# Kernel tuning notes

Hardware: AMD Instinct MI355X
Metric: run time of the kernel (lower is better)

The kernel has to match this reference:

```python
import jax, jax.numpy as jnp
import numpy as np

EPS = 1e-5

def _fftfreq(n, d):
    k = jnp.concatenate([jnp.arange(0, (n + 1) // 2), jnp.arange(-(n // 2), 0)]).astype(jnp.float32)
    return k / (n * d)

def _inorm(x):
    # InstanceNorm2d, no affine, biased variance, eps=1e-5; x: (B,C,H,W)
    m = jnp.mean(x, axis=(-2, -1), keepdims=True)
    v = jnp.var(x, axis=(-2, -1), keepdims=True)
    return (x - m) / jnp.sqrt(v + EPS)

def _spectral_conv(x, t_grid, x_grid, p1, p2, res):
    # x: (B, C, Sx, Sy) real; p1:(in,out,m1) p2:(in,out,m2) res:(in,out,m1,m2) complex64
    B, C, Sx, Sy = x.shape
    dty = x_grid[0, 1] - x_grid[0, 0]
    dtx = t_grid[0, 1] - t_grid[0, 0]
    alpha = jnp.fft.fft2(x, axes=(-2, -1))  # (B,in,Sx,Sy) complex
    om1 = (_fftfreq(Sx, dty) * (2 * jnp.pi) * 1j).astype(jnp.complex64)  # (Sx,)
    om2 = (_fftfreq(Sy, dtx) * (2 * jnp.pi) * 1j).astype(jnp.complex64)  # (Sy,)
    d1 = om1[:, None, None, None] - p1  # (Sx,in,out,m1)
    d2 = om2[:, None, None, None] - p2  # (Sy,in,out,m2)
    denom = jnp.einsum('pbix,qbik->pqbixk', d1, d2)  # (Sx,Sy,in,out,m1,m2)
    Hw = res[None, None] / denom  # pole-residue rational kernel
    r1 = jnp.einsum('biox,oxikpq->bkox', alpha, Hw)  # (B,out,Sx,Sy)
    r2 = jnp.einsum('biox,oxikpq->bkpq', alpha, Hw)  # (B,out,m1,m2)
    x1 = jnp.real(jnp.fft.ifft2(r1, s=(Sx, Sy), axes=(-2, -1)))
    ty_c = x_grid.reshape(1, -1).astype(jnp.complex64)  # (1,Sx)
    tx_c = t_grid.reshape(1, -1).astype(jnp.complex64)  # (1,Sy)
    e1 = jnp.exp(jnp.einsum('bip,kz->bipz', p1, ty_c))  # (in,out,m1,Sx)
    e2 = jnp.exp(jnp.einsum('biq,kx->biqx', p2, tx_c))  # (in,out,m2,Sy)
    term3 = jnp.einsum('bipz,biqx->bipqzx', e1, e2)     # (in,out,m1,m2,Sx,Sy)
    x2 = jnp.real(jnp.einsum('kbpq,bipqzx->kizx', r2, term3)) / (Sx * Sy)
    return x1 + x2

def reference(x, fc0_w, fc0_b, p1r, p1i, p2r, p2i, resr, resi,
              w0_w, w0_b, fc1_w, fc1_b, fc2_w, fc2_b, t_grid, x_grid):
    B, Sx, Sy, _ = x.shape
    gx = jnp.broadcast_to(jnp.linspace(0.0, 1.0, Sx, dtype=jnp.float32)[None, :, None, None], (B, Sx, Sy, 1))
    gy = jnp.broadcast_to(jnp.linspace(0.0, 1.0, Sy, dtype=jnp.float32)[None, None, :, None], (B, Sx, Sy, 1))
    h = jnp.concatenate([x, gx, gy], axis=-1)           # (B,Sx,Sy,3)
    h = h @ fc0_w.T + fc0_b                              # (B,Sx,Sy,16)
    h = h.transpose(0, 3, 1, 2)                          # (B,16,Sx,Sy)
    p1 = (p1r + 1j * p1i).astype(jnp.complex64)
    p2 = (p2r + 1j * p2i).astype(jnp.complex64)
    res = (resr + 1j * resi).astype(jnp.complex64)
    x1 = _inorm(_spectral_conv(_inorm(h), t_grid, x_grid, p1, p2, res))
    x2 = jnp.einsum('bihw,oi->bohw', h, w0_w) + w0_b[None, :, None, None]  # 1x1 conv
    h = x1 + x2
    h = h.transpose(0, 2, 3, 1)                          # (B,Sx,Sy,16)
    h = jnp.sin(h @ fc1_w.T + fc1_b)                     # (B,Sx,Sy,128)
    h = h @ fc2_w.T + fc2_b                              # (B,Sx,Sy,1)
    return h

def setup_inputs() -> dict:
    key = jax.random.key(0)
    ks = jax.random.split(key, 16)
    W, M1, M2, B, S = 16, 4, 5, 4, 64
    scale = 1.0 / (W * W)
    inp = {
        'x': jax.random.normal(ks[0], (B, S, S, 1), jnp.float32),
        'fc0_w': jax.random.normal(ks[1], (W, 3), jnp.float32) * 0.3,
        'fc0_b': jax.random.normal(ks[2], (W,), jnp.float32) * 0.1,
        'p1r': jax.random.uniform(ks[3], (W, W, M1), jnp.float32) * scale,
        'p1i': jax.random.uniform(ks[4], (W, W, M1), jnp.float32) * scale,
        'p2r': jax.random.uniform(ks[5], (W, W, M2), jnp.float32) * scale,
        'p2i': jax.random.uniform(ks[6], (W, W, M2), jnp.float32) * scale,
        'resr': jax.random.uniform(ks[7], (W, W, M1, M2), jnp.float32) * scale,
        'resi': jax.random.uniform(ks[8], (W, W, M1, M2), jnp.float32) * scale,
        'w0_w': jax.random.normal(ks[9], (W, W), jnp.float32) * 0.25,
        'w0_b': jax.random.normal(ks[10], (W,), jnp.float32) * 0.1,
        'fc1_w': jax.random.normal(ks[11], (128, W), jnp.float32) * 0.25,
        'fc1_b': jax.random.normal(ks[12], (128,), jnp.float32) * 0.1,
        'fc2_w': jax.random.normal(ks[13], (1, 128), jnp.float32) * 0.1,
        'fc2_b': jax.random.normal(ks[14], (1,), jnp.float32) * 0.1,
        't_grid': jnp.linspace(0.0, 1.0, S, dtype=jnp.float32).reshape(1, S),
        'x_grid': jnp.linspace(0.0, 1.0, S, dtype=jnp.float32).reshape(1, S),
    }
    return inp
```

## Files before the change

### kernel.cpp

```cpp
#include <hip/hip_runtime.h>

typedef float2 cplx;

constexpr int NPIX = 4096;
constexpr float TWO_PI = 6.28318530717958647692f;

__device__ inline void cmac(float& ax, float& ay, cplx a, cplx b) {
    ax += a.x * b.x - a.y * b.y;
    ay += a.x * b.y + a.y * b.x;
}

__global__ __launch_bounds__(256) void k_pre(
    const float* __restrict__ p1r, const float* __restrict__ p1i,
    const float* __restrict__ p2r, const float* __restrict__ p2i,
    const float* __restrict__ resr, const float* __restrict__ resi,
    const float* __restrict__ t_grid, const float* __restrict__ x_grid,
    cplx* __restrict__ A, cplx* __restrict__ Bq, cplx* __restrict__ Cq,
    cplx* __restrict__ e1, cplx* __restrict__ e2)
{
    int idx = blockIdx.x * 256 + threadIdx.x;
    float dty = x_grid[1] - x_grid[0];
    float dtx = t_grid[1] - t_grid[0];
    const int NA = 65536, NBQ = 81920, NCQ = 81920, NE1 = 65536;
    if (idx < NA) {
        int p = idx & 3, k = (idx >> 2) & 15, i = (idx >> 6) & 15, o = idx >> 10;
        int kf = (o < 32) ? o : o - 64;
        float om = TWO_PI * (float)kf / (64.f * dty);
        float dr = -p1r[(i * 16 + k) * 4 + p], di = om - p1i[(i * 16 + k) * 4 + p];
        float inv = 1.f / (dr * dr + di * di);
        A[idx] = make_float2(dr * inv, -di * inv);
        return;
    }
    idx -= NA;
    if (idx < NBQ) {
        int q = idx % 5, k = (idx / 5) & 15, i = (idx / 80) & 15, xx = idx / 1280;
        int kf = (xx < 32) ? xx : xx - 64;
        float om = TWO_PI * (float)kf / (64.f * dtx);
        float dr = -p2r[(i * 16 + k) * 5 + q], di = om - p2i[(i * 16 + k) * 5 + q];
        float inv = 1.f / (dr * dr + di * di);
        Bq[idx] = make_float2(dr * inv, -di * inv);
        return;
    }
    idx -= NBQ;
    if (idx < NCQ) {
        int q = idx % 5, k = (idx / 5) & 15, i = (idx / 80) & 15, o = idx / 1280;
        int kf = (o < 32) ? o : o - 64;
        float om = TWO_PI * (float)kf / (64.f * dty);
        float cx = 0.f, cy = 0.f;
        for (int p = 0; p < 4; ++p) {
            float dr = -p1r[(i * 16 + k) * 4 + p], di = om - p1i[(i * 16 + k) * 4 + p];
            float inv = 1.f / (dr * dr + di * di);
            float axr = dr * inv, axi = -di * inv;
            float rr = resr[((i * 16 + k) * 4 + p) * 5 + q];
            float ri = resi[((i * 16 + k) * 4 + p) * 5 + q];
            cx += rr * axr - ri * axi;
            cy += rr * axi + ri * axr;
        }
        Cq[idx] = make_float2(cx, cy);
        return;
    }
    idx -= NCQ;
    if (idx < NE1) {
        int z = idx & 63, w = idx >> 6;
        float t = x_grid[z];
        float m = expf(p1r[w] * t);
        float sn, cs; sincosf(p1i[w] * t, &sn, &cs);
        e1[idx] = make_float2(m * cs, m * sn);
        return;
    }
    idx -= NE1;
    {
        int xx = idx & 63, w = idx >> 6;
        float t = t_grid[xx];
        float m = expf(p2r[w] * t);
        float sn, cs; sincosf(p2i[w] * t, &sn, &cs);
        e2[idx] = make_float2(m * cs, m * sn);
    }
}

__global__ __launch_bounds__(1024) void k1_h_norm_fftA(
    const float* __restrict__ x, const float* __restrict__ fc0_w,
    const float* __restrict__ fc0_b, float* __restrict__ h, cplx* __restrict__ T1)
{
    __shared__ float tile[4096];
    __shared__ float rs[32];
    __shared__ cplx Ws[64];
    int bc = blockIdx.x, b = bc >> 4, c = bc & 15;
    int tid = threadIdx.x;
    if (tid < 64) { float sn, cs; sincosf(-TWO_PI * tid / 64.f, &sn, &cs); Ws[tid] = make_float2(cs, sn); }
    float w0 = fc0_w[c * 3], w1 = fc0_w[c * 3 + 1], w2 = fc0_w[c * 3 + 2], bb = fc0_b[c];
    const float inv63 = 1.f / 63.f;
    float vals[4]; float s = 0.f;
    for (int t = 0; t < 4; ++t) {
        int pix = t * 1024 + tid; int z = pix >> 6, xx = pix & 63;
        float v = w0 * x[b * 4096 + pix] + w1 * (z * inv63) + w2 * (xx * inv63) + bb;
        vals[t] = v; s += v; h[bc * 4096 + pix] = v;
    }
    for (int m = 32; m; m >>= 1) s += __shfl_xor(s, m, 64);
    if ((tid & 63) == 0) rs[tid >> 6] = s;
    __syncthreads();
    if (tid == 0) { float t0 = 0; for (int w = 0; w < 16; ++w) t0 += rs[w]; rs[16] = t0; }
    __syncthreads();
    float mean = rs[16] * (1.f / 4096.f);
    float s2 = 0.f;
    for (int t = 0; t < 4; ++t) { float d = vals[t] - mean; s2 += d * d; }
    for (int m = 32; m; m >>= 1) s2 += __shfl_xor(s2, m, 64);
    __syncthreads();
    if ((tid & 63) == 0) rs[tid >> 6] = s2;
    __syncthreads();
    if (tid == 0) { float t0 = 0; for (int w = 0; w < 16; ++w) t0 += rs[w]; rs[16] = t0; }
    __syncthreads();
    float rstd = rsqrtf(rs[16] * (1.f / 4096.f) + 1e-5f);
    for (int t = 0; t < 4; ++t) { int pix = t * 1024 + tid; tile[pix] = (vals[t] - mean) * rstd; }
    __syncthreads();
    int j = tid & 63, pl = tid >> 6;
    for (int t = 0; t < 4; ++t) {
        int p = pl + t * 16;
        float ax = 0.f, ay = 0.f;
        #pragma unroll 8
        for (int i = 0; i < 64; ++i) {
            float v = tile[i * 64 + j];
            cplx w = Ws[(p * i) & 63];
            ax += v * w.x; ay += v * w.y;
        }
        T1[bc * 4096 + p * 64 + j] = make_float2(ax, ay);
    }
}

__global__ __launch_bounds__(256) void k2_fftB(
    const cplx* __restrict__ T1, cplx* __restrict__ alpha, cplx* __restrict__ alphaT)
{
    __shared__ cplx T1s[256];
    __shared__ cplx Ws[64];
    int bc = blockIdx.x >> 4, pc = blockIdx.x & 15;
    int tid = threadIdx.x;
    if (tid < 64) { float sn, cs; sincosf(-TWO_PI * tid / 64.f, &sn, &cs); Ws[tid] = make_float2(cs, sn); }
    T1s[tid] = T1[bc * 4096 + pc * 256 + tid];
    __syncthreads();
    int q = tid & 63, pl = tid >> 6, p = pc * 4 + pl;
    float ax = 0.f, ay = 0.f;
    #pragma unroll 8
    for (int j = 0; j < 64; ++j) cmac(ax, ay, T1s[pl * 64 + j], Ws[(q * j) & 63]);
    cplx v = make_float2(ax, ay);
    alpha [bc * 4096 + p * 64 + q] = v;
    alphaT[(p * 64 + q) * 64 + bc] = v;
}

__global__ __launch_bounds__(64) void k3_r1(
    const cplx* __restrict__ alphaT, const cplx* __restrict__ Cq,
    const cplx* __restrict__ Bq, cplx* __restrict__ r1)
{
    __shared__ cplx Cqs[1280], Bqs[1280], Gs[256], as[64];
    int ox = blockIdx.x; int o = ox >> 6, xx = ox & 63;
    int t = threadIdx.x;
    for (int m = 0; m < 20; ++m) {
        Cqs[m * 64 + t] = Cq[o * 1280 + m * 64 + t];
        Bqs[m * 64 + t] = Bq[xx * 1280 + m * 64 + t];
    }
    as[t] = alphaT[ox * 64 + t];
    __syncthreads();
    for (int m = 0; m < 4; ++m) {
        int e = m * 64 + t; int i = e >> 4, k = e & 15;
        float gx = 0.f, gy = 0.f;
        for (int q = 0; q < 5; ++q) cmac(gx, gy, Cqs[i * 80 + k * 5 + q], Bqs[i * 80 + k * 5 + q]);
        Gs[e] = make_float2(gx, gy);
    }
    __syncthreads();
    int b = t >> 4, k = t & 15;
    float ax = 0.f, ay = 0.f;
    for (int i = 0; i < 16; ++i) cmac(ax, ay, as[b * 16 + i], Gs[i * 16 + k]);
    r1[t * 4096 + ox] = make_float2(ax, ay);
}

__global__ __launch_bounds__(256) void k4_inner1(
    const cplx* __restrict__ alpha, const cplx* __restrict__ Bq,
    cplx* __restrict__ inner1)
{
    int idx = blockIdx.x * 256 + threadIdx.x;
    int kq = idx % 80; int r = idx / 80; int o = r & 63; int bi = r >> 6; int i = bi & 15;
    const cplx* arow = alpha + bi * 4096 + o * 64;
    const cplx* bcol = Bq + i * 80 + kq;
    float ax = 0.f, ay = 0.f;
    #pragma unroll 4
    for (int x = 0; x < 64; ++x) cmac(ax, ay, arow[x], bcol[x * 1280]);
    inner1[idx] = make_float2(ax, ay);
}

__global__ __launch_bounds__(64) void k5_r2(
    const cplx* __restrict__ A, const cplx* __restrict__ inner1,
    const float* __restrict__ resr, const float* __restrict__ resi,
    cplx* __restrict__ r2)
{
    int bk = blockIdx.x; int b = bk >> 4, k = bk & 15;
    int o = threadIdx.x;
    float accx[4][5] = {}, accy[4][5] = {};
    for (int i = 0; i < 16; ++i) {
        cplx a[4];
        for (int p = 0; p < 4; ++p) a[p] = A[((o * 16 + i) * 16 + k) * 4 + p];
        cplx in[5];
        for (int q = 0; q < 5; ++q) in[q] = inner1[(b * 16 + i) * 5120 + o * 80 + k * 5 + q];
        int rb = (i * 16 + k) * 20;
        for (int p = 0; p < 4; ++p)
            for (int q = 0; q < 5; ++q) {
                float tx = a[p].x * in[q].x - a[p].y * in[q].y;
                float ty = a[p].x * in[q].y + a[p].y * in[q].x;
                float rr = resr[rb + p * 5 + q], ri = resi[rb + p * 5 + q];
                accx[p][q] += rr * tx - ri * ty;
                accy[p][q] += rr * ty + ri * tx;
            }
    }
    for (int m = 32; m; m >>= 1)
        for (int p = 0; p < 4; ++p)
            for (int q = 0; q < 5; ++q) {
                accx[p][q] += __shfl_xor(accx[p][q], m, 64);
                accy[p][q] += __shfl_xor(accy[p][q], m, 64);
            }
    if (o == 0)
        for (int p = 0; p < 4; ++p)
            for (int q = 0; q < 5; ++q)
                r2[bk * 20 + p * 5 + q] = make_float2(accx[p][q], accy[p][q]);
}

__global__ __launch_bounds__(256) void k6_V(
    const cplx* __restrict__ r2, const cplx* __restrict__ e1, cplx* __restrict__ V)
{
    int idx = blockIdx.x * 256 + threadIdx.x;
    int z = idx & 63;
    int rest = idx >> 6;
    int q = rest % 5; rest /= 5;
    int bb = rest & 15; rest >>= 4;
    int i = rest & 15;
    int kb = rest >> 4;
    float vx = 0.f, vy = 0.f;
    for (int p = 0; p < 4; ++p)
        cmac(vx, vy, r2[((kb * 16 + bb) * 4 + p) * 5 + q],
                     e1[((bb * 16 + i) * 4 + p) * 64 + z]);
    V[idx] = make_float2(vx, vy);
}

__global__ __launch_bounds__(256) void k7_ifftA(
    const cplx* __restrict__ r1, cplx* __restrict__ T2)
{
    __shared__ cplx Ws[64];
    int bk = blockIdx.x >> 4, zc = blockIdx.x & 15;
    int tid = threadIdx.x;
    if (tid < 64) { float sn, cs; sincosf(TWO_PI * tid / 64.f, &sn, &cs); Ws[tid] = make_float2(cs, sn); }
    __syncthreads();
    int j = tid & 63, z = zc * 4 + (tid >> 6);
    const cplx* rr = r1 + bk * 4096 + j;
    float ax = 0.f, ay = 0.f;
    #pragma unroll 4
    for (int o = 0; o < 64; ++o) cmac(ax, ay, rr[o * 64], Ws[(z * o) & 63]);
    T2[bk * 4096 + z * 64 + j] = make_float2(ax, ay);
}

__global__ __launch_bounds__(1024) void k8_sp(
    const cplx* __restrict__ T2, const cplx* __restrict__ V,
    const cplx* __restrict__ e2, float* __restrict__ spn)
{
    __shared__ cplx Es[5120];
    __shared__ float rs[32];
    __shared__ cplx Ws[64];
    int blk = blockIdx.x;
    int ch = blk & 15;
    int tid = threadIdx.x;
    if (tid < 64) { float sn, cs; sincosf(TWO_PI * tid / 64.f, &sn, &cs); Ws[tid] = make_float2(cs, sn); }
    for (int t = 0; t < 5; ++t) {
        int f = t * 1024 + tid; int xx = f & 63, bq = f >> 6; int bb = bq / 5, q = bq % 5;
        Es[f] = e2[((bb * 16 + ch) * 5 + q) * 64 + xx];
    }
    __syncthreads();
    const cplx* T2b = T2 + blk * 4096;
    const cplx* Vb  = V  + blk * 5120;
    int xx = tid & 63;
    float vals[4]; float s = 0.f;
    for (int t = 0; t < 4; ++t) {
        int pix = t * 1024 + tid; int z = pix >> 6;
        float acc = 0.f;
        const cplx* trow = T2b + z * 64;
        #pragma unroll 4
        for (int j2 = 0; j2 < 64; ++j2) {
            cplx v = trow[j2]; cplx w = Ws[(xx * j2) & 63];
            acc += v.x * w.x - v.y * w.y;
        }
        #pragma unroll 4
        for (int bq = 0; bq < 80; ++bq) {
            cplx vv = Vb[bq * 64 + z];
            cplx ee = Es[bq * 64 + xx];
            acc += vv.x * ee.x - vv.y * ee.y;
        }
        float val = acc * (1.f / 4096.f);
        vals[t] = val; s += val;
    }
    for (int m = 32; m; m >>= 1) s += __shfl_xor(s, m, 64);
    if ((tid & 63) == 0) rs[tid >> 6] = s;
    __syncthreads();
    if (tid == 0) { float t0 = 0; for (int w = 0; w < 16; ++w) t0 += rs[w]; rs[16] = t0; }
    __syncthreads();
    float mean = rs[16] * (1.f / 4096.f);
    float s2 = 0.f;
    for (int t = 0; t < 4; ++t) { float d = vals[t] - mean; s2 += d * d; }
    for (int m = 32; m; m >>= 1) s2 += __shfl_xor(s2, m, 64);
    __syncthreads();
    if ((tid & 63) == 0) rs[tid >> 6] = s2;
    __syncthreads();
    if (tid == 0) { float t0 = 0; for (int w = 0; w < 16; ++w) t0 += rs[w]; rs[16] = t0; }
    __syncthreads();
    float rstd = rsqrtf(rs[16] * (1.f / 4096.f) + 1e-5f);
    for (int t = 0; t < 4; ++t) {
        int pix = t * 1024 + tid;
        spn[blk * 4096 + pix] = (vals[t] - mean) * rstd;
    }
}

__global__ __launch_bounds__(256) void k9_final(
    const float* __restrict__ spn, const float* __restrict__ h,
    const float* __restrict__ w0_w, const float* __restrict__ w0_b,
    const float* __restrict__ fc1_w, const float* __restrict__ fc1_b,
    const float* __restrict__ fc2_w, const float* __restrict__ fc2_b,
    float* __restrict__ out)
{
    __shared__ float w1s[128 * 16], b1s[128], w2s[128], w0s[256], w0bs[16];
    int tid = threadIdx.x;
    for (int t = 0; t < 8; ++t) w1s[t * 256 + tid] = fc1_w[t * 256 + tid];
    if (tid < 128) { b1s[tid] = fc1_b[tid]; w2s[tid] = fc2_w[tid]; }
    w0s[tid] = w0_w[tid & 255];
    if (tid < 16) w0bs[tid] = w0_b[tid];
    float b2 = fc2_b[0];
    __syncthreads();
    int pix = blockIdx.x * 256 + tid;
    int b = pix >> 12, rem = pix & 4095;
    float hv[16], tv[16];
    for (int c = 0; c < 16; ++c) {
        hv[c] = h[(b * 16 + c) * 4096 + rem];
        tv[c] = spn[(b * 16 + c) * 4096 + rem];
    }
    for (int k = 0; k < 16; ++k) {
        float a = w0bs[k];
        for (int c = 0; c < 16; ++c) a += w0s[k * 16 + c] * hv[c];
        tv[k] += a;
    }
    float acc = b2;
    for (int n = 0; n < 128; ++n) {
        float s1 = b1s[n];
        for (int k2 = 0; k2 < 16; ++k2) s1 += w1s[n * 16 + k2] * tv[k2];
        acc += w2s[n] * sinf(s1);
    }
    out[pix] = acc;
}

extern "C" void kernel_launch(void* const* d_in, const int* in_sizes, int n_in,
                              void* d_out, int out_size, void* d_ws, size_t ws_size,
                              hipStream_t stream)
{
    const float* x     = (const float*)d_in[0];
    const float* fc0_w = (const float*)d_in[1];
    const float* fc0_b = (const float*)d_in[2];
    const float* p1r   = (const float*)d_in[3];
    const float* p1i   = (const float*)d_in[4];
    const float* p2r   = (const float*)d_in[5];
    const float* p2i   = (const float*)d_in[6];
    const float* resr  = (const float*)d_in[7];
    const float* resi  = (const float*)d_in[8];
    const float* w0_w  = (const float*)d_in[9];
    const float* w0_b  = (const float*)d_in[10];
    const float* fc1_w = (const float*)d_in[11];
    const float* fc1_b = (const float*)d_in[12];
    const float* fc2_w = (const float*)d_in[13];
    const float* fc2_b = (const float*)d_in[14];
    const float* t_grid= (const float*)d_in[15];
    const float* x_grid= (const float*)d_in[16];
    float* out = (float*)d_out;

    float* ws = (float*)d_ws;
    size_t off = 0;
    float* h      = ws + off; off += 262144;
    cplx*  T1     = (cplx*)(ws + off); off += 524288;
    cplx*  alpha  = (cplx*)(ws + off); off += 524288;
    cplx*  alphaT = (cplx*)(ws + off); off += 524288;
    cplx*  A      = (cplx*)(ws + off); off += 131072;
    cplx*  Bq     = (cplx*)(ws + off); off += 163840;
    cplx*  Cq     = (cplx*)(ws + off); off += 163840;
    cplx*  e1     = (cplx*)(ws + off); off += 131072;
    cplx*  e2     = (cplx*)(ws + off); off += 163840;
    cplx*  r1     = (cplx*)(ws + off); off += 524288;
    cplx*  inner1 = (cplx*)(ws + off); off += 655360;
    cplx*  r2     = (cplx*)(ws + off); off += 2560;
    cplx*  V      = (cplx*)(ws + off); off += 655360;
    cplx*  T2     = (cplx*)(ws + off); off += 524288;
    float* spn    = ws + off; off += 262144;
    (void)ws_size; (void)n_in; (void)in_sizes; (void)out_size;

    k_pre<<<1472, 256, 0, stream>>>(p1r, p1i, p2r, p2i, resr, resi, t_grid, x_grid,
                                    A, Bq, Cq, e1, e2);
    k1_h_norm_fftA<<<64, 1024, 0, stream>>>(x, fc0_w, fc0_b, h, T1);
    k2_fftB<<<1024, 256, 0, stream>>>(T1, alpha, alphaT);
    k3_r1<<<4096, 64, 0, stream>>>(alphaT, Cq, Bq, r1);
    k4_inner1<<<1280, 256, 0, stream>>>(alpha, Bq, inner1);
    k5_r2<<<64, 64, 0, stream>>>(A, inner1, resr, resi, r2);
    k6_V<<<1280, 256, 0, stream>>>(r2, e1, V);
    k7_ifftA<<<1024, 256, 0, stream>>>(r1, T2);
    k8_sp<<<64, 1024, 0, stream>>>(T2, V, e2, spn);
    k9_final<<<64, 256, 0, stream>>>(spn, h, w0_w, w0_b, fc1_w, fc1_b, fc2_w, fc2_b, out);
}
```

Measured before the change: 251.4 us.

## Split instance-norm stats into atomic reductions to widen fftA and sp grids

```diff
diff --git a/kernel.cpp b/kernel.cpp
--- a/kernel.cpp
+++ b/kernel.cpp
@@ -2,7 +2,6 @@
 
 typedef float2 cplx;
 
-constexpr int NPIX = 4096;
 constexpr float TWO_PI = 6.28318530717958647692f;
 
 __device__ inline void cmac(float& ax, float& ay, cplx a, cplx b) {
@@ -11,17 +10,20 @@
 }
 
 __global__ __launch_bounds__(256) void k_pre(
+    const float* __restrict__ x, const float* __restrict__ fc0_w,
+    const float* __restrict__ fc0_b,
     const float* __restrict__ p1r, const float* __restrict__ p1i,
     const float* __restrict__ p2r, const float* __restrict__ p2i,
     const float* __restrict__ resr, const float* __restrict__ resi,
     const float* __restrict__ t_grid, const float* __restrict__ x_grid,
     cplx* __restrict__ A, cplx* __restrict__ Bq, cplx* __restrict__ Cq,
-    cplx* __restrict__ e1, cplx* __restrict__ e2)
+    cplx* __restrict__ e1, cplx* __restrict__ e2,
+    float* __restrict__ h, float* __restrict__ accH)
 {
     int idx = blockIdx.x * 256 + threadIdx.x;
     float dty = x_grid[1] - x_grid[0];
     float dtx = t_grid[1] - t_grid[0];
-    const int NA = 65536, NBQ = 81920, NCQ = 81920, NE1 = 65536;
+    const int NA = 65536, NBQ = 81920, NCQ = 81920, NE1 = 65536, NE2 = 81920;
     if (idx < NA) {
         int p = idx & 3, k = (idx >> 2) & 15, i = (idx >> 6) & 15, o = idx >> 10;
         int kf = (o < 32) ? o : o - 64;
@@ -69,62 +71,59 @@
         return;
     }
     idx -= NE1;
-    {
+    if (idx < NE2) {
         int xx = idx & 63, w = idx >> 6;
         float t = t_grid[xx];
         float m = expf(p2r[w] * t);
         float sn, cs; sincosf(p2i[w] * t, &sn, &cs);
         e2[idx] = make_float2(m * cs, m * sn);
-    }
-}
-
-__global__ __launch_bounds__(1024) void k1_h_norm_fftA(
-    const float* __restrict__ x, const float* __restrict__ fc0_w,
-    const float* __restrict__ fc0_b, float* __restrict__ h, cplx* __restrict__ T1)
-{
-    __shared__ float tile[4096];
-    __shared__ float rs[32];
+        return;
+    }
+    idx -= NE2;
+    {
+        int bc = idx >> 12, pix = idx & 4095;
+        int b = bc >> 4, c = bc & 15;
+        int z = pix >> 6, xx = pix & 63;
+        const float inv63 = 1.f / 63.f;
+        float v = fc0_w[c * 3] * x[b * 4096 + pix]
+                + fc0_w[c * 3 + 1] * (z * inv63)
+                + fc0_w[c * 3 + 2] * (xx * inv63) + fc0_b[c];
+        h[idx] = v;
+        float s = v, s2 = v * v;
+        for (int m = 32; m; m >>= 1) {
+            s  += __shfl_xor(s,  m, 64);
+            s2 += __shfl_xor(s2, m, 64);
+        }
+        if ((threadIdx.x & 63) == 0) {
+            atomicAdd(&accH[bc * 2],     s);
+            atomicAdd(&accH[bc * 2 + 1], s2);
+        }
+    }
+}
+
+__global__ __launch_bounds__(256) void k_fftA(
+    const float* __restrict__ h, const float* __restrict__ accH,
+    cplx* __restrict__ T1)
+{
     __shared__ cplx Ws[64];
-    int bc = blockIdx.x, b = bc >> 4, c = bc & 15;
+    int bc = blockIdx.x >> 4, pc = blockIdx.x & 15;
     int tid = threadIdx.x;
     if (tid < 64) { float sn, cs; sincosf(-TWO_PI * tid / 64.f, &sn, &cs); Ws[tid] = make_float2(cs, sn); }
-    float w0 = fc0_w[c * 3], w1 = fc0_w[c * 3 + 1], w2 = fc0_w[c * 3 + 2], bb = fc0_b[c];
-    const float inv63 = 1.f / 63.f;
-    float vals[4]; float s = 0.f;
-    for (int t = 0; t < 4; ++t) {
-        int pix = t * 1024 + tid; int z = pix >> 6, xx = pix & 63;
-        float v = w0 * x[b * 4096 + pix] + w1 * (z * inv63) + w2 * (xx * inv63) + bb;
-        vals[t] = v; s += v; h[bc * 4096 + pix] = v;
-    }
-    for (int m = 32; m; m >>= 1) s += __shfl_xor(s, m, 64);
-    if ((tid & 63) == 0) rs[tid >> 6] = s;
-    __syncthreads();
-    if (tid == 0) { float t0 = 0; for (int w = 0; w < 16; ++w) t0 += rs[w]; rs[16] = t0; }
-    __syncthreads();
-    float mean = rs[16] * (1.f / 4096.f);
-    float s2 = 0.f;
-    for (int t = 0; t < 4; ++t) { float d = vals[t] - mean; s2 += d * d; }
-    for (int m = 32; m; m >>= 1) s2 += __shfl_xor(s2, m, 64);
-    __syncthreads();
-    if ((tid & 63) == 0) rs[tid >> 6] = s2;
-    __syncthreads();
-    if (tid == 0) { float t0 = 0; for (int w = 0; w < 16; ++w) t0 += rs[w]; rs[16] = t0; }
-    __syncthreads();
-    float rstd = rsqrtf(rs[16] * (1.f / 4096.f) + 1e-5f);
-    for (int t = 0; t < 4; ++t) { int pix = t * 1024 + tid; tile[pix] = (vals[t] - mean) * rstd; }
-    __syncthreads();
-    int j = tid & 63, pl = tid >> 6;
-    for (int t = 0; t < 4; ++t) {
-        int p = pl + t * 16;
-        float ax = 0.f, ay = 0.f;
-        #pragma unroll 8
-        for (int i = 0; i < 64; ++i) {
-            float v = tile[i * 64 + j];
-            cplx w = Ws[(p * i) & 63];
-            ax += v * w.x; ay += v * w.y;
-        }
-        T1[bc * 4096 + p * 64 + j] = make_float2(ax, ay);
-    }
+    __syncthreads();
+    float mean = accH[bc * 2] * (1.f / 4096.f);
+    float var  = accH[bc * 2 + 1] * (1.f / 4096.f) - mean * mean;
+    float rstd = rsqrtf(var + 1e-5f);
+    int j = tid & 63, pl = tid >> 6, p = pc * 4 + pl;
+    const float* hb = h + bc * 4096 + j;
+    float ax = 0.f, ay = 0.f;
+    #pragma unroll 8
+    for (int i = 0; i < 64; ++i) {
+        float v = hb[i * 64];
+        cplx w = Ws[(p * i) & 63];
+        ax += v * w.x; ay += v * w.y;
+    }
+    if (p == 0) ax -= 64.f * mean;
+    T1[bc * 4096 + p * 64 + j] = make_float2(ax * rstd, ay * rstd);
 }
 
 __global__ __launch_bounds__(256) void k2_fftB(
@@ -254,86 +253,77 @@
     T2[bk * 4096 + z * 64 + j] = make_float2(ax, ay);
 }
 
-__global__ __launch_bounds__(1024) void k8_sp(
+__global__ __launch_bounds__(256) void k8a_sp(
     const cplx* __restrict__ T2, const cplx* __restrict__ V,
-    const cplx* __restrict__ e2, float* __restrict__ spn)
-{
-    __shared__ cplx Es[5120];
-    __shared__ float rs[32];
+    const cplx* __restrict__ e2, float* __restrict__ sp, float* __restrict__ accS)
+{
     __shared__ cplx Ws[64];
-    int blk = blockIdx.x;
-    int ch = blk & 15;
+    int bc = blockIdx.x >> 4, zc = blockIdx.x & 15;
+    int ch = bc & 15;
     int tid = threadIdx.x;
     if (tid < 64) { float sn, cs; sincosf(TWO_PI * tid / 64.f, &sn, &cs); Ws[tid] = make_float2(cs, sn); }
-    for (int t = 0; t < 5; ++t) {
-        int f = t * 1024 + tid; int xx = f & 63, bq = f >> 6; int bb = bq / 5, q = bq % 5;
-        Es[f] = e2[((bb * 16 + ch) * 5 + q) * 64 + xx];
-    }
-    __syncthreads();
-    const cplx* T2b = T2 + blk * 4096;
-    const cplx* Vb  = V  + blk * 5120;
-    int xx = tid & 63;
-    float vals[4]; float s = 0.f;
-    for (int t = 0; t < 4; ++t) {
-        int pix = t * 1024 + tid; int z = pix >> 6;
-        float acc = 0.f;
-        const cplx* trow = T2b + z * 64;
-        #pragma unroll 4
-        for (int j2 = 0; j2 < 64; ++j2) {
-            cplx v = trow[j2]; cplx w = Ws[(xx * j2) & 63];
-            acc += v.x * w.x - v.y * w.y;
-        }
-        #pragma unroll 4
-        for (int bq = 0; bq < 80; ++bq) {
-            cplx vv = Vb[bq * 64 + z];
-            cplx ee = Es[bq * 64 + xx];
+    __syncthreads();
+    int lp = zc * 256 + tid;
+    int z = lp >> 6, xx = lp & 63;
+    const cplx* trow = T2 + bc * 4096 + z * 64;
+    const cplx* Vb   = V + bc * 5120;
+    const cplx* eb   = e2 + ch * 320 + xx;
+    float acc = 0.f;
+    #pragma unroll 8
+    for (int j = 0; j < 64; ++j) {
+        cplx v = trow[j]; cplx w = Ws[(xx * j) & 63];
+        acc += v.x * w.x - v.y * w.y;
+    }
+    #pragma unroll 4
+    for (int bb = 0; bb < 16; ++bb)
+        for (int q = 0; q < 5; ++q) {
+            cplx vv = Vb[bb * 320 + q * 64 + z];
+            cplx ee = eb[bb * 5120 + q * 64];
             acc += vv.x * ee.x - vv.y * ee.y;
         }
-        float val = acc * (1.f / 4096.f);
-        vals[t] = val; s += val;
-    }
-    for (int m = 32; m; m >>= 1) s += __shfl_xor(s, m, 64);
-    if ((tid & 63) == 0) rs[tid >> 6] = s;
-    __syncthreads();
-    if (tid == 0) { float t0 = 0; for (int w = 0; w < 16; ++w) t0 += rs[w]; rs[16] = t0; }
-    __syncthreads();
-    float mean = rs[16] * (1.f / 4096.f);
-    float s2 = 0.f;
-    for (int t = 0; t < 4; ++t) { float d = vals[t] - mean; s2 += d * d; }
-    for (int m = 32; m; m >>= 1) s2 += __shfl_xor(s2, m, 64);
-    __syncthreads();
-    if ((tid & 63) == 0) rs[tid >> 6] = s2;
-    __syncthreads();
-    if (tid == 0) { float t0 = 0; for (int w = 0; w < 16; ++w) t0 += rs[w]; rs[16] = t0; }
-    __syncthreads();
-    float rstd = rsqrtf(rs[16] * (1.f / 4096.f) + 1e-5f);
-    for (int t = 0; t < 4; ++t) {
-        int pix = t * 1024 + tid;
-        spn[blk * 4096 + pix] = (vals[t] - mean) * rstd;
+    float val = acc * (1.f / 4096.f);
+    sp[bc * 4096 + lp] = val;
+    float s = val, s2 = val * val;
+    for (int m = 32; m; m >>= 1) {
+        s  += __shfl_xor(s,  m, 64);
+        s2 += __shfl_xor(s2, m, 64);
+    }
+    if ((tid & 63) == 0) {
+        atomicAdd(&accS[bc * 2],     s);
+        atomicAdd(&accS[bc * 2 + 1], s2);
     }
 }
 
 __global__ __launch_bounds__(256) void k9_final(
-    const float* __restrict__ spn, const float* __restrict__ h,
+    const float* __restrict__ sp, const float* __restrict__ accS,
+    const float* __restrict__ h,
     const float* __restrict__ w0_w, const float* __restrict__ w0_b,
     const float* __restrict__ fc1_w, const float* __restrict__ fc1_b,
     const float* __restrict__ fc2_w, const float* __restrict__ fc2_b,
     float* __restrict__ out)
 {
     __shared__ float w1s[128 * 16], b1s[128], w2s[128], w0s[256], w0bs[16];
-    int tid = threadIdx.x;
+    __shared__ float mvm[16], mvr[16];
+    int tid = threadIdx.x;
+    int b = blockIdx.x >> 4;
     for (int t = 0; t < 8; ++t) w1s[t * 256 + tid] = fc1_w[t * 256 + tid];
     if (tid < 128) { b1s[tid] = fc1_b[tid]; w2s[tid] = fc2_w[tid]; }
     w0s[tid] = w0_w[tid & 255];
-    if (tid < 16) w0bs[tid] = w0_b[tid];
+    if (tid < 16) {
+        w0bs[tid] = w0_b[tid];
+        float mean = accS[(b * 16 + tid) * 2] * (1.f / 4096.f);
+        float var  = accS[(b * 16 + tid) * 2 + 1] * (1.f / 4096.f) - mean * mean;
+        mvm[tid] = mean;
+        mvr[tid] = rsqrtf(var + 1e-5f);
+    }
     float b2 = fc2_b[0];
     __syncthreads();
     int pix = blockIdx.x * 256 + tid;
-    int b = pix >> 12, rem = pix & 4095;
+    int rem = pix & 4095;
     float hv[16], tv[16];
     for (int c = 0; c < 16; ++c) {
         hv[c] = h[(b * 16 + c) * 4096 + rem];
-        tv[c] = spn[(b * 16 + c) * 4096 + rem];
+        tv[c] = (sp[(b * 16 + c) * 4096 + rem] - mvm[c]) * mvr[c];
     }
     for (int k = 0; k < 16; ++k) {
         float a = w0bs[k];
@@ -388,18 +378,22 @@
     cplx*  r2     = (cplx*)(ws + off); off += 2560;
     cplx*  V      = (cplx*)(ws + off); off += 655360;
     cplx*  T2     = (cplx*)(ws + off); off += 524288;
-    float* spn    = ws + off; off += 262144;
+    float* sp     = ws + off; off += 262144;
+    float* accum  = ws + off; off += 256;
+    float* accH = accum, *accS = accum + 128;
     (void)ws_size; (void)n_in; (void)in_sizes; (void)out_size;
 
-    k_pre<<<1472, 256, 0, stream>>>(p1r, p1i, p2r, p2i, resr, resi, t_grid, x_grid,
-                                    A, Bq, Cq, e1, e2);
-    k1_h_norm_fftA<<<64, 1024, 0, stream>>>(x, fc0_w, fc0_b, h, T1);
+    hipMemsetAsync(accum, 0, 256 * sizeof(float), stream);
+
+    k_pre<<<2496, 256, 0, stream>>>(x, fc0_w, fc0_b, p1r, p1i, p2r, p2i, resr, resi,
+                                    t_grid, x_grid, A, Bq, Cq, e1, e2, h, accH);
+    k_fftA<<<1024, 256, 0, stream>>>(h, accH, T1);
     k2_fftB<<<1024, 256, 0, stream>>>(T1, alpha, alphaT);
     k3_r1<<<4096, 64, 0, stream>>>(alphaT, Cq, Bq, r1);
     k4_inner1<<<1280, 256, 0, stream>>>(alpha, Bq, inner1);
     k5_r2<<<64, 64, 0, stream>>>(A, inner1, resr, resi, r2);
     k6_V<<<1280, 256, 0, stream>>>(r2, e1, V);
     k7_ifftA<<<1024, 256, 0, stream>>>(r1, T2);
-    k8_sp<<<64, 1024, 0, stream>>>(T2, V, e2, spn);
-    k9_final<<<64, 256, 0, stream>>>(spn, h, w0_w, w0_b, fc1_w, fc1_b, fc2_w, fc2_b, out);
-}
+    k8a_sp<<<1024, 256, 0, stream>>>(T2, V, e2, sp, accS);
+    k9_final<<<64, 256, 0, stream>>>(sp, accS, h, w0_w, w0_b, fc1_w, fc1_b, fc2_w, fc2_b, out);
+}
```

Result: slower. 261.6 us (+4.0%).
